# Performance work log

Measured on AMD Instinct MI355X. Metric: run time of the kernel, lower is better.

## Reference

```python
import jax, jax.numpy as jnp
import numpy as np

N_NODES = 100000
N_EDGES = 1600000
IN_FEATS = 128
HIDDEN = 128
NUM_CLASSES = 64


def setup_inputs() -> dict:
    key = jax.random.key(0)
    k1, k2, k3, k4, k5 = jax.random.split(key, 5)
    inputs = jax.random.normal(k1, (N_NODES, IN_FEATS), dtype=jnp.float32)
    src = jax.random.randint(k2, (N_EDGES,), 0, N_NODES, dtype=jnp.int32)
    dst = jax.random.randint(k3, (N_EDGES,), 0, N_NODES, dtype=jnp.int32)
    W1 = jax.random.normal(k4, (IN_FEATS, HIDDEN), dtype=jnp.float32) / np.sqrt(IN_FEATS)
    b1 = jnp.zeros((HIDDEN,), dtype=jnp.float32)
    W2 = jax.random.normal(k5, (HIDDEN, NUM_CLASSES), dtype=jnp.float32) / np.sqrt(HIDDEN)
    b2 = jnp.zeros((NUM_CLASSES,), dtype=jnp.float32)
    return {"inputs": inputs, "src": src, "dst": dst, "W1": W1, "b1": b1, "W2": W2, "b2": b2}


def _graph_conv(x, src, dst, W, b, n_nodes):
    # DGL GraphConv, norm='both': h = D_in^{-1/2} A D_out^{-1/2} x W + b
    ones = jnp.ones(src.shape[0], dtype=x.dtype)
    deg_out = jax.ops.segment_sum(ones, src, num_segments=n_nodes)
    deg_in = jax.ops.segment_sum(ones, dst, num_segments=n_nodes)
    norm_src = jax.lax.rsqrt(jnp.clip(deg_out, 1.0))  # [N]
    norm_dst = jax.lax.rsqrt(jnp.clip(deg_in, 1.0))   # [N]
    x = x * norm_src[:, None]
    msgs = x[src]                                      # [E, d] gather
    agg = jax.ops.segment_sum(msgs, dst, num_segments=n_nodes)  # [N, d] scatter-add
    agg = agg * norm_dst[:, None]
    return agg @ W + b


def reference(inputs, src, dst, W1, b1, W2, b2):
    n = inputs.shape[0]
    h = _graph_conv(inputs, src, dst, W1, b1, n)
    h = jax.nn.relu(h)
    h = _graph_conv(h, src, dst, W2, b2, n)
    return h
```

## Files before the change

kernel.cpp:

```cpp
#include <hip/hip_runtime.h>
#include <hip/hip_bf16.h>

#define N_FEATS_IN 128
#define BK_BITS 8
#define BK_SIZE 256
#define EPB 4096
#define MAXNB 512

typedef _Float16 h8 __attribute__((ext_vector_type(8)));
typedef float    f4v __attribute__((ext_vector_type(4)));
typedef float    f8v __attribute__((ext_vector_type(8)));

__device__ inline int wave_incl_scan(int v) {
    const int lane = threadIdx.x & 63;
    for (int off = 1; off < 64; off <<= 1) {
        int u = __shfl_up(v, off, 64);
        if (lane >= off) v += u;
    }
    return v;
}

__device__ inline int block_excl_scan(int s, int* ws, int* total) {
    const int lane = threadIdx.x & 63, wid = threadIdx.x >> 6;
    int inc = wave_incl_scan(s);
    if (lane == 63) ws[wid] = inc;
    __syncthreads();
    int woff = 0;
#pragma unroll
    for (int w = 0; w < 4; ++w) woff += (w < wid) ? ws[w] : 0;
    if (total) *total = ws[0] + ws[1] + ws[2] + ws[3];
    return woff + inc - s;
}

__global__ __launch_bounds__(256) void hist_kernel(
    const int* __restrict__ src, const int* __restrict__ dst,
    int* __restrict__ bh_d, int* __restrict__ bh_s,
    const float* __restrict__ W1, const float* __restrict__ W2,
    _Float16* __restrict__ wf1g, _Float16* __restrict__ wf2g,
    int E, int NB) {
    __shared__ int hd[MAXNB];
    __shared__ int hs[MAXNB];
    const int t = threadIdx.x;

    const int widx = blockIdx.x * 256 + t;
    if (widx < 128 * 128) {
        const int i = widx;
        const int k = i >> 7, c = i & 127;
        const int tt = c >> 4, s = k >> 5, q = (k >> 3) & 3, j = k & 7;
        wf1g[(((tt * 4 + s) * 4 + q) * 16 + (c & 15)) * 8 + j] =
            (_Float16)W1[i];
    } else if (widx < 128 * 128 + 128 * 64) {
        const int i = widx - 128 * 128;
        const int k = i >> 6, c = i & 63;
        const int tt = c >> 4, s = k >> 5, q = (k >> 3) & 3, j = k & 7;
        wf2g[(((tt * 4 + s) * 4 + q) * 16 + (c & 15)) * 8 + j] =
            (_Float16)W2[i];
    }

    for (int i = t; i < NB; i += 256) { hd[i] = 0; hs[i] = 0; }
    __syncthreads();
    const int base = blockIdx.x * EPB;
    const int end = min(base + EPB, E);
    for (int e = base + t; e < end; e += 256) {
        atomicAdd(&hd[dst[e] >> BK_BITS], 1);
        atomicAdd(&hs[src[e] >> BK_BITS], 1);
    }
    __syncthreads();
    for (int i = t; i < NB; i += 256) {
        bh_d[(size_t)blockIdx.x * NB + i] = hd[i];
        bh_s[(size_t)blockIdx.x * NB + i] = hs[i];
    }
}

__global__ __launch_bounds__(256) void colprefix2_kernel(
    int* __restrict__ bh_d, int* __restrict__ bh_s,
    int* __restrict__ tot_d, int* __restrict__ tot_s, int NBLK, int NB) {
    __shared__ int ws[4];
    const int b = blockIdx.x;
    const int t = threadIdx.x;
    int carry = 0;
    for (int base = 0; base < NBLK; base += 256) {
        const int r = base + t;
        const int v = (r < NBLK) ? bh_d[(size_t)r * NB + b] : 0;
        int total;
        const int e = block_excl_scan(v, ws, &total);
        if (r < NBLK) bh_d[(size_t)r * NB + b] = carry + e;
        carry += total;
        __syncthreads();
    }
    if (t == 0) tot_d[b] = carry;
    carry = 0;
    for (int base = 0; base < NBLK; base += 256) {
        const int r = base + t;
        const int v = (r < NBLK) ? bh_s[(size_t)r * NB + b] : 0;
        int total;
        const int e = block_excl_scan(v, ws, &total);
        if (r < NBLK) bh_s[(size_t)r * NB + b] = carry + e;
        carry += total;
        __syncthreads();
    }
    if (t == 0) tot_s[b] = carry;
}

__global__ __launch_bounds__(256) void bscan2_kernel(
    const int* __restrict__ tot_d, const int* __restrict__ tot_s,
    int* __restrict__ gb_d, int* __restrict__ gb_s,
    int* __restrict__ row_ptr, int NB, int N, int E) {
    __shared__ int ws[4];
    const int t = threadIdx.x;
    const int i0 = t * 4;
    {
        int a[4];
#pragma unroll
        for (int u = 0; u < 4; ++u) a[u] = (i0 + u < NB) ? tot_d[i0 + u] : 0;
        int e0 = block_excl_scan(a[0] + a[1] + a[2] + a[3], ws, nullptr);
#pragma unroll
        for (int u = 0; u < 4; ++u) {
            if (i0 + u < NB) gb_d[i0 + u] = e0;
            e0 += a[u];
        }
    }
    __syncthreads();
    {
        int a[4];
#pragma unroll
        for (int u = 0; u < 4; ++u) a[u] = (i0 + u < NB) ? tot_s[i0 + u] : 0;
        int e0 = block_excl_scan(a[0] + a[1] + a[2] + a[3], ws, nullptr);
#pragma unroll
        for (int u = 0; u < 4; ++u) {
            if (i0 + u < NB) gb_s[i0 + u] = e0;
            e0 += a[u];
        }
    }
    if (t == 0) { gb_d[NB] = E; gb_s[NB] = E; row_ptr[N] = E; }
}

__global__ __launch_bounds__(256) void scatter2_kernel(
    const int* __restrict__ src, const int* __restrict__ dst,
    const int* __restrict__ bh_d, const int* __restrict__ bh_s,
    const int* __restrict__ gb_d, const int* __restrict__ gb_s,
    unsigned int* __restrict__ ebuf, unsigned char* __restrict__ sbuf,
    int E, int NB) {
    __shared__ int cd[MAXNB];
    __shared__ int cs[MAXNB];
    const int t = threadIdx.x;
    for (int i = t; i < NB; i += 256) {
        cd[i] = bh_d[(size_t)blockIdx.x * NB + i] + gb_d[i];
        cs[i] = bh_s[(size_t)blockIdx.x * NB + i] + gb_s[i];
    }
    __syncthreads();
    const int base = blockIdx.x * EPB;
    const int end = min(base + EPB, E);
    for (int e = base + t; e < end; e += 256) {
        const int d = dst[e];
        const int s = src[e];
        const int pd = atomicAdd(&cd[d >> BK_BITS], 1);
        ebuf[pd] = ((unsigned)s << 8) | (unsigned)(d & (BK_SIZE - 1));
        const int ps = atomicAdd(&cs[s >> BK_BITS], 1);
        sbuf[ps] = (unsigned char)(s & (BK_SIZE - 1));
    }
}

__global__ __launch_bounds__(256) void bucket_csr_kernel(
    const unsigned int* __restrict__ ebuf, const int* __restrict__ gb_d,
    const unsigned char* __restrict__ sbuf, const int* __restrict__ gb_s,
    int* __restrict__ row_ptr, float* __restrict__ norm_dst,
    float* __restrict__ norm_src, int* __restrict__ edge_src, int N) {
    __shared__ int cnt[BK_SIZE];
    __shared__ int lro[BK_SIZE];
    __shared__ int ws[4];
    const int b = blockIdx.x;
    const int t = threadIdx.x;
    const int beg = gb_d[b], end = gb_d[b + 1];
    const int node = b * BK_SIZE + t;

    cnt[t] = 0;
    __syncthreads();
    for (int j = beg + t; j < end; j += 256)
        atomicAdd(&cnt[ebuf[j] & (BK_SIZE - 1)], 1);
    __syncthreads();

    const int v = cnt[t];
    const int excl = block_excl_scan(v, ws, nullptr);
    lro[t] = beg + excl;
    if (node < N) {
        row_ptr[node] = beg + excl;
        norm_dst[node] = rsqrtf(fmaxf((float)v, 1.0f));
    }
    __syncthreads();
    cnt[t] = 0;
    __syncthreads();

    for (int j = beg + t; j < end; j += 256) {
        const unsigned int ed = ebuf[j];
        const int dl = ed & (BK_SIZE - 1);
        const int p = atomicAdd(&cnt[dl], 1);
        edge_src[lro[dl] + p] = (int)(ed >> 8);
    }

    __syncthreads();
    cnt[t] = 0;
    __syncthreads();
    const int sb = gb_s[b], se = gb_s[b + 1];
    for (int j = sb + t; j < se; j += 256)
        atomicAdd(&cnt[sbuf[j]], 1);
    __syncthreads();
    if (node < N)
        norm_src[node] = rsqrtf(fmaxf((float)cnt[t], 1.0f));
}

template <int OC, bool XHALF>
__global__ __launch_bounds__(256) void mfma_gemm_kernel(
    const void* __restrict__ Xv, const _Float16* __restrict__ Wg,
    const float* __restrict__ scale, _Float16* __restrict__ Y, int n) {
    constexpr int K = 128;
    constexpr int NT = OC / 16;
    constexpr int RPB = 128;
    __shared__ _Float16 Wf[NT * 4 * 64 * 8];

    const int tid = threadIdx.x;
    for (int i = tid * 8; i < K * OC; i += 256 * 8)
        *(h8*)&Wf[i] = *(const h8*)&Wg[i];
    __syncthreads();

    const int lane = tid & 63;
    const int wv = tid >> 6;
    const int m = lane & 15, q = lane >> 4;

#pragma unroll
    for (int it = 0; it < RPB / 64; ++it) {
        const int rbase = blockIdx.x * RPB + it * 64 + wv * 16;
        const int lrow = min(rbase + m, n - 1);

        h8 a[4];
        if constexpr (XHALF) {
            const _Float16* X = (const _Float16*)Xv;
            const _Float16* p = &X[(size_t)lrow * K + q * 8];
#pragma unroll
            for (int s = 0; s < 4; ++s) a[s] = *(const h8*)(p + s * 32);
        } else {
            const float* X = (const float*)Xv;
            const float* p = &X[(size_t)lrow * K + q * 8];
#pragma unroll
            for (int s = 0; s < 4; ++s) {
                const float4 u0 = *(const float4*)(p + s * 32);
                const float4 u1 = *(const float4*)(p + s * 32 + 4);
                h8 v;
                v[0] = (_Float16)u0.x; v[1] = (_Float16)u0.y;
                v[2] = (_Float16)u0.z; v[3] = (_Float16)u0.w;
                v[4] = (_Float16)u1.x; v[5] = (_Float16)u1.y;
                v[6] = (_Float16)u1.z; v[7] = (_Float16)u1.w;
                a[s] = v;
            }
        }

        f4v acc[NT];
#pragma unroll
        for (int t = 0; t < NT; ++t) acc[t] = (f4v)0.0f;

#pragma unroll
        for (int s = 0; s < 4; ++s) {
#pragma unroll
            for (int t = 0; t < NT; ++t) {
                const h8 b = *(const h8*)&Wf[((t * 4 + s) * 64 + lane) * 8];
                acc[t] = __builtin_amdgcn_mfma_f32_16x16x32_f16(
                    a[s], b, acc[t], 0, 0, 0);
            }
        }

#pragma unroll
        for (int r = 0; r < 4; ++r) {
            const int orow = rbase + q * 4 + r;
            if (orow < n) {
                const float sc = scale[orow];
#pragma unroll
                for (int t = 0; t < NT; ++t)
                    Y[(size_t)orow * OC + t * 16 + m] =
                        (_Float16)(acc[t][r] * sc);
            }
        }
    }
}

template <int TPN>
__device__ inline f8v gather_rows(const h8* __restrict__ T8,
                                  const int* __restrict__ edge_src,
                                  int beg, int end, int f8) {
    f8v acc = (f8v)0.0f;
    int j = beg;
    for (; j + 15 < end; j += 16) {
        int s[16];
#pragma unroll
        for (int u = 0; u < 16; ++u) s[u] = edge_src[j + u];
        h8 a[16];
#pragma unroll
        for (int u = 0; u < 16; ++u) a[u] = T8[(size_t)s[u] * TPN + f8];
#pragma unroll
        for (int u = 0; u < 16; ++u)
            acc += __builtin_convertvector(a[u], f8v);
    }
    for (; j + 7 < end; j += 8) {
        int s[8];
#pragma unroll
        for (int u = 0; u < 8; ++u) s[u] = edge_src[j + u];
        h8 a[8];
#pragma unroll
        for (int u = 0; u < 8; ++u) a[u] = T8[(size_t)s[u] * TPN + f8];
#pragma unroll
        for (int u = 0; u < 8; ++u)
            acc += __builtin_convertvector(a[u], f8v);
    }
    for (; j + 3 < end; j += 4) {
        int s[4];
#pragma unroll
        for (int u = 0; u < 4; ++u) s[u] = edge_src[j + u];
        h8 a[4];
#pragma unroll
        for (int u = 0; u < 4; ++u) a[u] = T8[(size_t)s[u] * TPN + f8];
#pragma unroll
        for (int u = 0; u < 4; ++u)
            acc += __builtin_convertvector(a[u], f8v);
    }
    for (; j < end; ++j)
        acc += __builtin_convertvector(T8[(size_t)edge_src[j] * TPN + f8], f8v);
    return acc;
}

template <int FEAT, bool RELU, bool OUT_HALF>
__global__ __launch_bounds__(256) void gather_agg_kernel(
    const _Float16* __restrict__ T, const int* __restrict__ row_ptr,
    const int* __restrict__ edge_src, const float* __restrict__ norm_dst,
    const float* __restrict__ bias, void* __restrict__ outv, int n) {
    constexpr int TPN = FEAT / 8;
    constexpr int NPB = 256 / TPN;
    const int node = blockIdx.x * NPB + threadIdx.x / TPN;
    const int f8 = threadIdx.x % TPN;
    if (node >= n) return;
    const int beg = row_ptr[node];
    const int end = row_ptr[node + 1];

    f8v acc = gather_rows<TPN>((const h8*)T, edge_src, beg, end, f8);

    const float nd = norm_dst[node];
    float r[8];
#pragma unroll
    for (int k = 0; k < 8; ++k) {
        r[k] = acc[k] * nd + bias[f8 * 8 + k];
        if constexpr (RELU) r[k] = fmaxf(r[k], 0.0f);
    }

    if constexpr (OUT_HALF) {
        _Float16* out = (_Float16*)outv;
        h8 o;
#pragma unroll
        for (int k = 0; k < 8; ++k) o[k] = (_Float16)r[k];
        *(h8*)&out[(size_t)node * FEAT + f8 * 8] = o;
    } else {
        float* out = (float*)outv;
        float4 o0 = make_float4(r[0], r[1], r[2], r[3]);
        float4 o1 = make_float4(r[4], r[5], r[6], r[7]);
        *(float4*)&out[(size_t)node * FEAT + f8 * 8] = o0;
        *(float4*)&out[(size_t)node * FEAT + f8 * 8 + 4] = o1;
    }
}

template <int FEAT, int OC>
__global__ __launch_bounds__(256) void gather_gemm_kernel(
    const _Float16* __restrict__ T, const int* __restrict__ row_ptr,
    const int* __restrict__ edge_src, const float* __restrict__ norm_dst,
    const float* __restrict__ norm_src, const float* __restrict__ bias,
    const _Float16* __restrict__ Wg, _Float16* __restrict__ Y, int n) {
    constexpr int TPN = FEAT / 8;
    constexpr int NPB = 256 / TPN;
    constexpr int AP = FEAT + 8;
    __shared__ _Float16 Ah[NPB * AP];

    const int tid = threadIdx.x;
    const int node = blockIdx.x * NPB + tid / TPN;
    const int f8 = tid % TPN;
    const int nl = tid / TPN;

    float r[8];
    if (node < n) {
        const int beg = row_ptr[node];
        const int end = row_ptr[node + 1];
        f8v acc = gather_rows<TPN>((const h8*)T, edge_src, beg, end, f8);

        const float nd = norm_dst[node];
        const float ns = norm_src[node];
#pragma unroll
        for (int k = 0; k < 8; ++k) {
            float v = acc[k] * nd + bias[f8 * 8 + k];
            v = fmaxf(v, 0.0f);
            r[k] = v * ns;
        }
    } else {
#pragma unroll
        for (int k = 0; k < 8; ++k) r[k] = 0.0f;
    }

    {
        h8 av;
#pragma unroll
        for (int k = 0; k < 8; ++k) av[k] = (_Float16)r[k];
        *(h8*)&Ah[nl * AP + f8 * 8] = av;
    }
    __syncthreads();

    const int lane = tid & 63, w = tid >> 6;
    const int m = lane & 15, q = lane >> 4;
    f4v acc2 = (f4v)0.0f;
#pragma unroll
    for (int s = 0; s < 4; ++s) {
        const h8 a = *(const h8*)&Ah[m * AP + s * 32 + q * 8];
        const h8 b = *(const h8*)&Wg[((w * 4 + s) * 64 + lane) * 8];
        acc2 = __builtin_amdgcn_mfma_f32_16x16x32_f16(a, b, acc2, 0, 0, 0);
    }
#pragma unroll
    for (int rr = 0; rr < 4; ++rr) {
        const int orow = blockIdx.x * NPB + q * 4 + rr;
        if (orow < n)
            Y[(size_t)orow * OC + w * 16 + m] = (_Float16)acc2[rr];
    }
}

extern "C" void kernel_launch(void* const* d_in, const int* in_sizes, int n_in,
                              void* d_out, int out_size, void* d_ws, size_t ws_size,
                              hipStream_t stream) {
    const float* x   = (const float*)d_in[0];
    const int*   src = (const int*)d_in[1];
    const int*   dst = (const int*)d_in[2];
    const float* W1  = (const float*)d_in[3];
    const float* b1  = (const float*)d_in[4];
    const float* W2  = (const float*)d_in[5];
    const float* b2  = (const float*)d_in[6];
    float* out = (float*)d_out;

    const int N = in_sizes[0] / N_FEATS_IN;
    const int E = in_sizes[1];
    const int NB = (N + BK_SIZE - 1) / BK_SIZE;
    const int NBLK = (E + EPB - 1) / EPB;

    auto align4 = [](size_t w) { return (w + 3) & ~(size_t)3; };
    char* base = (char*)d_ws;
    size_t off = 0;
    auto take = [&](size_t words) {
        char* p = base + off * 4;
        off = align4(off + words);
        return p;
    };
    int*   tot_d    = (int*)take(NB);
    int*   tot_s    = (int*)take(NB);
    int*   gb_d     = (int*)take(NB + 1);
    int*   gb_s     = (int*)take(NB + 1);
    int*   bh_d     = (int*)take((size_t)NBLK * NB);
    int*   bh_s     = (int*)take((size_t)NBLK * NB);
    unsigned int*  ebuf = (unsigned int*)take(E);
    unsigned char* sbuf = (unsigned char*)take((E + 3) / 4);
    int*   row_ptr  = (int*)take(N + 1);
    int*   edge_src = (int*)take(E);
    float* norms    = (float*)take(2 * (size_t)N);
    _Float16* t1    = (_Float16*)take((size_t)N * 64);
    _Float16* t2    = (_Float16*)take((size_t)N * 32);
    _Float16* wf1g  = (_Float16*)take(128 * 128 / 2);
    _Float16* wf2g  = (_Float16*)take(128 * 64 / 2);
    float* norm_src = norms;
    float* norm_dst = norms + N;

    hist_kernel<<<NBLK, 256, 0, stream>>>(src, dst, bh_d, bh_s,
                                          W1, W2, wf1g, wf2g, E, NB);
    colprefix2_kernel<<<NB, 256, 0, stream>>>(bh_d, bh_s, tot_d, tot_s,
                                              NBLK, NB);
    bscan2_kernel<<<1, 256, 0, stream>>>(tot_d, tot_s, gb_d, gb_s, row_ptr,
                                         NB, N, E);
    scatter2_kernel<<<NBLK, 256, 0, stream>>>(src, dst, bh_d, bh_s, gb_d, gb_s,
                                              ebuf, sbuf, E, NB);
    bucket_csr_kernel<<<NB, 256, 0, stream>>>(ebuf, gb_d, sbuf, gb_s, row_ptr,
                                              norm_dst, norm_src, edge_src, N);

    mfma_gemm_kernel<128, false><<<(N + 127) / 128, 256, 0, stream>>>(
        x, wf1g, norm_src, t1, N);

    gather_gemm_kernel<128, 64><<<(N + 15) / 16, 256, 0, stream>>>(
        t1, row_ptr, edge_src, norm_dst, norm_src, b1, wf2g, t2, N);

    gather_agg_kernel<64, false, false><<<(N + 31) / 32, 256, 0, stream>>>(
        t2, row_ptr, edge_src, norm_dst, b2, out, N);
}
```

Measured before the change: 313.0 us.

## Stage bucket scatter in LDS for contiguous global writes

The scatter kernel now does a local counting sort of each block's 4096 edges in shared memory, by dst bucket and then by src bucket. Sorted values and their destination indices are staged in LDS, then written out linearly so that consecutive threads write consecutive addresses within a bucket run. Before, each edge was written to a scattered global position, which gave uncoalesced writes. The change costs about 32KB more LDS, several extra barriers and a block scan per pass, and it lowers occupancy.

After: 298.7 us. 1.05x faster.

```diff
diff --git a/kernel.cpp b/kernel.cpp
--- a/kernel.cpp
+++ b/kernel.cpp
@@ -141,24 +141,96 @@
     const int* __restrict__ gb_d, const int* __restrict__ gb_s,
     unsigned int* __restrict__ ebuf, unsigned char* __restrict__ sbuf,
     int E, int NB) {
-    __shared__ int cd[MAXNB];
-    __shared__ int cs[MAXNB];
+    __shared__ unsigned int eb_val[EPB];
+    __shared__ int eb_dst[EPB];
+    __shared__ int cur[MAXNB];
+    __shared__ int bd[MAXNB];
+    __shared__ int ws[4];
     const int t = threadIdx.x;
-    for (int i = t; i < NB; i += 256) {
-        cd[i] = bh_d[(size_t)blockIdx.x * NB + i] + gb_d[i];
-        cs[i] = bh_s[(size_t)blockIdx.x * NB + i] + gb_s[i];
-    }
-    __syncthreads();
     const int base = blockIdx.x * EPB;
     const int end = min(base + EPB, E);
-    for (int e = base + t; e < end; e += 256) {
-        const int d = dst[e];
-        const int s = src[e];
-        const int pd = atomicAdd(&cd[d >> BK_BITS], 1);
-        ebuf[pd] = ((unsigned)s << 8) | (unsigned)(d & (BK_SIZE - 1));
-        const int ps = atomicAdd(&cs[s >> BK_BITS], 1);
-        sbuf[ps] = (unsigned char)(s & (BK_SIZE - 1));
-    }
+    const int tot = end - base;
+    constexpr int ITER = EPB / 256;
+
+    unsigned sv[ITER];
+    int dv[ITER];
+    for (int i = t; i < MAXNB; i += 256) cur[i] = 0;
+    __syncthreads();
+#pragma unroll
+    for (int u = 0; u < ITER; ++u) {
+        const int e = base + t + u * 256;
+        if (e < end) {
+            sv[u] = (unsigned)src[e];
+            dv[u] = dst[e];
+            atomicAdd(&cur[dv[u] >> BK_BITS], 1);
+        } else {
+            dv[u] = -1;
+            sv[u] = 0;
+        }
+    }
+    __syncthreads();
+
+    {
+        const int i0 = 2 * t, i1 = 2 * t + 1;
+        const int a = cur[i0], b = cur[i1];
+        const int e0 = block_excl_scan(a + b, ws, nullptr);
+        const int g0 = (i0 < NB)
+            ? gb_d[i0] + bh_d[(size_t)blockIdx.x * NB + i0] : 0;
+        const int g1 = (i1 < NB)
+            ? gb_d[i1] + bh_d[(size_t)blockIdx.x * NB + i1] : 0;
+        cur[i0] = e0;
+        cur[i1] = e0 + a;
+        bd[i0] = g0 - e0;
+        bd[i1] = g1 - (e0 + a);
+    }
+    __syncthreads();
+#pragma unroll
+    for (int u = 0; u < ITER; ++u) {
+        if (dv[u] >= 0) {
+            const int b = dv[u] >> BK_BITS;
+            const int pos = atomicAdd(&cur[b], 1);
+            eb_val[pos] = (sv[u] << 8) | (unsigned)(dv[u] & (BK_SIZE - 1));
+            eb_dst[pos] = bd[b] + pos;
+        }
+    }
+    __syncthreads();
+    for (int i = t; i < tot; i += 256)
+        ebuf[eb_dst[i]] = eb_val[i];
+    __syncthreads();
+
+    for (int i = t; i < MAXNB; i += 256) cur[i] = 0;
+    __syncthreads();
+#pragma unroll
+    for (int u = 0; u < ITER; ++u)
+        if (dv[u] >= 0) atomicAdd(&cur[(int)(sv[u] >> BK_BITS)], 1);
+    __syncthreads();
+    {
+        const int i0 = 2 * t, i1 = 2 * t + 1;
+        const int a = cur[i0], b = cur[i1];
+        const int e0 = block_excl_scan(a + b, ws, nullptr);
+        const int g0 = (i0 < NB)
+            ? gb_s[i0] + bh_s[(size_t)blockIdx.x * NB + i0] : 0;
+        const int g1 = (i1 < NB)
+            ? gb_s[i1] + bh_s[(size_t)blockIdx.x * NB + i1] : 0;
+        cur[i0] = e0;
+        cur[i1] = e0 + a;
+        bd[i0] = g0 - e0;
+        bd[i1] = g1 - (e0 + a);
+    }
+    __syncthreads();
+    unsigned char* sb_val = (unsigned char*)eb_val;
+#pragma unroll
+    for (int u = 0; u < ITER; ++u) {
+        if (dv[u] >= 0) {
+            const int b = (int)(sv[u] >> BK_BITS);
+            const int pos = atomicAdd(&cur[b], 1);
+            sb_val[pos] = (unsigned char)(sv[u] & (BK_SIZE - 1));
+            eb_dst[pos] = bd[b] + pos;
+        }
+    }
+    __syncthreads();
+    for (int i = t; i < tot; i += 256)
+        sbuf[eb_dst[i]] = sb_val[i];
 }
 
 __global__ __launch_bounds__(256) void bucket_csr_kernel(
```
